# Performance work log

Measured on AMD Instinct MI355X. Metric: run time of the kernel, lower is better.

The kernel has to match this reference:

```python
import jax, jax.numpy as jnp
import numpy as np

IN_FEATURES = 256
OUT_FEATURES = 512
NUM_SEGMENTS = 8
GRID_MIN, GRID_MAX = -1.0, 1.0
STEP = (GRID_MAX - GRID_MIN) / NUM_SEGMENTS
LN_EPS = 1e-5


def setup_inputs() -> dict:
    key = jax.random.key(0)
    k1, k2 = jax.random.split(key)
    B = 2048
    x = jax.random.normal(k1, (B, IN_FEATURES), dtype=jnp.float32)
    # Xavier-uniform a_embed, zeros b_embed, as in reset_parameters
    vocab = IN_FEATURES * NUM_SEGMENTS
    limit = float(np.sqrt(6.0 / (vocab + OUT_FEATURES)))
    a_weight = jax.random.uniform(k2, (vocab, OUT_FEATURES), minval=-limit, maxval=limit, dtype=jnp.float32)
    b_weight = jnp.zeros((vocab, OUT_FEATURES), dtype=jnp.float32)
    gamma = jnp.ones((IN_FEATURES,), dtype=jnp.float32)
    beta = jnp.zeros((IN_FEATURES,), dtype=jnp.float32)
    return {"x": x, "a_weight": a_weight, "b_weight": b_weight, "gamma": gamma, "beta": beta}


def reference(x, a_weight, b_weight, gamma, beta):
    # LayerNorm over in_features
    mu = jnp.mean(x, axis=-1, keepdims=True)
    var = jnp.mean(jnp.square(x - mu), axis=-1, keepdims=True)
    xn = (x - mu) * jax.lax.rsqrt(var + LN_EPS) * gamma + beta  # [B, I]

    # data-dependent segment index (torch .long() truncates; clamp makes trunc==floor here)
    float_idx = (xn - GRID_MIN) / STEP
    seg = jnp.clip(float_idx.astype(jnp.int32), 0, NUM_SEGMENTS - 1)  # [B, I]
    global_idx = seg + jnp.arange(IN_FEATURES, dtype=jnp.int32)[None, :] * NUM_SEGMENTS

    a_vals = a_weight[global_idx]  # [B, I, O]
    b_vals = b_weight[global_idx]  # [B, I, O]
    # sum over in_features of a*x + b
    y = jnp.einsum('bi,bio->bo', xn, a_vals) + jnp.sum(b_vals, axis=1)
    return y
```

## Files before the change

kernel.cpp:

```cpp
#include <hip/hip_runtime.h>

#define I_FEAT 256
#define O_FEAT 512
#define NSEG   8
#define KDIM   (I_FEAT * NSEG)
#define KTOT   (2 * KDIM)
#define KC_N   (KTOT / 32)

typedef _Float16 half8   __attribute__((ext_vector_type(8)));
typedef float    floatx4 __attribute__((ext_vector_type(4)));
typedef uint32_t uintx4  __attribute__((ext_vector_type(4)));

__global__ __launch_bounds__(256) void prep(
    const float* __restrict__ x,
    const float* __restrict__ Aw,
    const float* __restrict__ Bw,
    const float* __restrict__ gamma,
    const float* __restrict__ beta,
    uint4* __restrict__ Bf,
    uint2* __restrict__ Am,
    int Bn, int pbTot)
{
    __shared__ char smem[16 * 260 * 4];
    const int t   = threadIdx.x;
    const int bid = blockIdx.x;

    if (bid < pbTot) {
        unsigned short (*T)[72] = (unsigned short(*)[72])smem;
        const int n0 = (bid & 7) * 64;
        const int k0 = (bid >> 3) * 64;
        const float* src = (k0 < KDIM) ? (Aw + (size_t)k0 * O_FEAT)
                                       : (Bw + (size_t)(k0 - KDIM) * O_FEAT);
        #pragma unroll
        for (int s = 0; s < 4; ++s) {
            int e  = s * 1024 + t * 4;
            int kl = e >> 6, nl = e & 63;
            const float4 v = *(const float4*)(src + (size_t)kl * O_FEAT + n0 + nl);
            T[nl + 0][kl] = __builtin_bit_cast(unsigned short, (_Float16)v.x);
            T[nl + 1][kl] = __builtin_bit_cast(unsigned short, (_Float16)v.y);
            T[nl + 2][kl] = __builtin_bit_cast(unsigned short, (_Float16)v.z);
            T[nl + 3][kl] = __builtin_bit_cast(unsigned short, (_Float16)v.w);
        }
        __syncthreads();

        const int lane = t & 63, lane16 = lane & 15, quad = lane >> 4;
        const int sub  = t >> 6;
        #pragma unroll
        for (int f = 0; f < 2; ++f) {
            const int combo = sub * 2 + f;
            const int n16g  = combo & 3;
            const int kch   = combo >> 2;
            const int nl = n16g * 16 + lane16;
            const int kl = kch * 32 + quad * 8;
            const uint4 val = *(const uint4*)&T[nl][kl];
            const int n16t = (n0 >> 4) + n16g;
            const int kc   = (k0 >> 5) + kch;
            Bf[((size_t)n16t * KC_N + kc) * 64 + lane] = val;
        }
    } else {
        uint32_t (*M)[260] = (uint32_t(*)[260])smem;
        const int mt16 = bid - pbTot;
        const int rr   = t >> 4;
        const int c16  = t & 15;
        const int row  = mt16 * 16 + rr;
        const bool ok  = (row < Bn);

        float4 v[4];
        const float* xr = x + (size_t)row * I_FEAT + c16 * 16;
        #pragma unroll
        for (int j = 0; j < 4; ++j)
            v[j] = ok ? *(const float4*)(xr + j * 4) : make_float4(0.f, 0.f, 0.f, 0.f);

        float sum = 0.f, sq = 0.f;
        #pragma unroll
        for (int j = 0; j < 4; ++j) {
            sum += v[j].x + v[j].y + v[j].z + v[j].w;
            sq  += v[j].x * v[j].x + v[j].y * v[j].y
                 + v[j].z * v[j].z + v[j].w * v[j].w;
        }
        #pragma unroll
        for (int mask = 1; mask < 16; mask <<= 1) {
            sum += __shfl_xor(sum, mask);
            sq  += __shfl_xor(sq,  mask);
        }
        const float mu  = sum * (1.0f / I_FEAT);
        const float var = sq * (1.0f / I_FEAT) - mu * mu;
        const float rs  = rsqrtf(var + 1e-5f);

        #pragma unroll
        for (int j = 0; j < 4; ++j) {
            const float4 g4 = *(const float4*)(gamma + c16 * 16 + j * 4);
            const float4 b4 = *(const float4*)(beta  + c16 * 16 + j * 4);
            const float vv[4] = { v[j].x, v[j].y, v[j].z, v[j].w };
            const float gg[4] = { g4.x, g4.y, g4.z, g4.w };
            const float bb[4] = { b4.x, b4.y, b4.z, b4.w };
            #pragma unroll
            for (int e = 0; e < 4; ++e) {
                const int c = c16 * 16 + j * 4 + e;
                float xn = (vv[e] - mu) * rs * gg[e] + bb[e];
                float fi = (xn + 1.0f) * 4.0f;
                int seg = (int)fi;
                seg = seg < 0 ? 0 : (seg > NSEG - 1 ? NSEG - 1 : seg);
                _Float16 hx = (_Float16)xn;
                M[rr][c] = ((uint32_t)seg << 16)
                         | (uint32_t)__builtin_bit_cast(unsigned short, hx);
            }
        }
        __syncthreads();

        const int lane = t & 63, g = t >> 6;
        const int m_local = lane & 15, quad = lane >> 4;
        uint2* dst = Am + (size_t)mt16 * 64 * 64 + lane;
        #pragma unroll
        for (int kk = 0; kk < 16; ++kk) {
            const int kcp = g * 16 + kk;
            const int w0  = kcp * 8 + quad;
            const int w1  = w0 + 4;
            const uint32_t u0 = M[m_local][w0 & 255];
            const uint32_t u1 = M[m_local][w1 & 255];
            const uint32_t a  = (w0 >> 8) ? ((u0 & 0xFFFF0000u) | 0x3C00u) : u0;
            const uint32_t b  = (w1 >> 8) ? ((u1 & 0xFFFF0000u) | 0x3C00u) : u1;
            dst[(size_t)kcp * 64] = make_uint2(a, b);
        }
    }
}

static __device__ __forceinline__ half8 build_onehot(uint32_t u) {
    const uint32_t xb  = u & 0xFFFFu;
    const uint32_t seg = u >> 16;
    const uint64_t oh  = (uint64_t)xb << ((seg & 3u) << 4);
    const uint64_t lo  = (seg < 4u) ? oh : 0ull;
    const uint64_t hi  = (seg < 4u) ? 0ull : oh;
    uintx4 w;
    w[0] = (uint32_t)lo; w[1] = (uint32_t)(lo >> 32);
    w[2] = (uint32_t)hi; w[3] = (uint32_t)(hi >> 32);
    return __builtin_bit_cast(half8, w);
}

__global__ __launch_bounds__(256, 2) void kan_gemm(
    const uint2* __restrict__ Am,
    const uint4* __restrict__ Bf,
    float* __restrict__ out,
    int Bn, int rt64Tot)
{
    __shared__ floatx4 s_red[4][8][64];

    const int t      = threadIdx.x;
    const int wave   = t >> 6, lane = t & 63;
    const int lane16 = lane & 15, quad = lane >> 4;
    const int bid    = blockIdx.x;

    int ot, rt;
    if (rt64Tot == 32) {
        const int xc = bid & 7, j = bid >> 3;
        ot = ((j >> 4) << 2) | (xc & 3);
        rt = (j & 15) | ((xc >> 2) << 4);
    } else {
        ot = bid & 15;
        rt = bid >> 4;
    }

    const uint2* pa = Am + (size_t)(rt * 4) * 64 * 64 + lane;
    const uint4* pb = Bf + (size_t)(ot * 2) * KC_N * 64 + lane;

    floatx4 acc[4][2] = {};
    const int kcp0 = wave * 16;

    #pragma unroll 4
    for (int p = 0; p < 16; ++p) {
        const int kcp = kcp0 + p;
        const uint2 u0 = pa[(size_t)kcp * 64];
        const uint2 u1 = pa[(size_t)(4096  + kcp * 64)];
        const uint2 u2 = pa[(size_t)(8192  + kcp * 64)];
        const uint2 u3 = pa[(size_t)(12288 + kcp * 64)];
        const uint4 b00 = pb[(size_t)(2 * kcp + 0) * 64];
        const uint4 b01 = pb[(size_t)(2 * kcp + 1) * 64];
        const uint4 b10 = pb[(size_t)(8192 + (2 * kcp + 0) * 64)];
        const uint4 b11 = pb[(size_t)(8192 + (2 * kcp + 1) * 64)];
        {
            const half8 n0 = __builtin_bit_cast(half8, b00);
            const half8 n1 = __builtin_bit_cast(half8, b10);
            half8 a;
            a = build_onehot(u0.x);
            acc[0][0] = __builtin_amdgcn_mfma_f32_16x16x32_f16(a, n0, acc[0][0], 0, 0, 0);
            acc[0][1] = __builtin_amdgcn_mfma_f32_16x16x32_f16(a, n1, acc[0][1], 0, 0, 0);
            a = build_onehot(u1.x);
            acc[1][0] = __builtin_amdgcn_mfma_f32_16x16x32_f16(a, n0, acc[1][0], 0, 0, 0);
            acc[1][1] = __builtin_amdgcn_mfma_f32_16x16x32_f16(a, n1, acc[1][1], 0, 0, 0);
            a = build_onehot(u2.x);
            acc[2][0] = __builtin_amdgcn_mfma_f32_16x16x32_f16(a, n0, acc[2][0], 0, 0, 0);
            acc[2][1] = __builtin_amdgcn_mfma_f32_16x16x32_f16(a, n1, acc[2][1], 0, 0, 0);
            a = build_onehot(u3.x);
            acc[3][0] = __builtin_amdgcn_mfma_f32_16x16x32_f16(a, n0, acc[3][0], 0, 0, 0);
            acc[3][1] = __builtin_amdgcn_mfma_f32_16x16x32_f16(a, n1, acc[3][1], 0, 0, 0);
        }
        {
            const half8 n0 = __builtin_bit_cast(half8, b01);
            const half8 n1 = __builtin_bit_cast(half8, b11);
            half8 a;
            a = build_onehot(u0.y);
            acc[0][0] = __builtin_amdgcn_mfma_f32_16x16x32_f16(a, n0, acc[0][0], 0, 0, 0);
            acc[0][1] = __builtin_amdgcn_mfma_f32_16x16x32_f16(a, n1, acc[0][1], 0, 0, 0);
            a = build_onehot(u1.y);
            acc[1][0] = __builtin_amdgcn_mfma_f32_16x16x32_f16(a, n0, acc[1][0], 0, 0, 0);
            acc[1][1] = __builtin_amdgcn_mfma_f32_16x16x32_f16(a, n1, acc[1][1], 0, 0, 0);
            a = build_onehot(u2.y);
            acc[2][0] = __builtin_amdgcn_mfma_f32_16x16x32_f16(a, n0, acc[2][0], 0, 0, 0);
            acc[2][1] = __builtin_amdgcn_mfma_f32_16x16x32_f16(a, n1, acc[2][1], 0, 0, 0);
            a = build_onehot(u3.y);
            acc[3][0] = __builtin_amdgcn_mfma_f32_16x16x32_f16(a, n0, acc[3][0], 0, 0, 0);
            acc[3][1] = __builtin_amdgcn_mfma_f32_16x16x32_f16(a, n1, acc[3][1], 0, 0, 0);
        }
    }

    #pragma unroll
    for (int mi = 0; mi < 4; ++mi)
        #pragma unroll
        for (int ni = 0; ni < 2; ++ni)
            s_red[wave][mi * 2 + ni][lane] = acc[mi][ni];
    __syncthreads();

    #pragma unroll
    for (int q = 0; q < 2; ++q) {
        const int tt = wave * 2 + q;
        const int mi = tt >> 1, ni = tt & 1;
        floatx4 vsum = s_red[0][tt][lane];
        vsum += s_red[1][tt][lane];
        vsum += s_red[2][tt][lane];
        vsum += s_red[3][tt][lane];
        const int gcol = ot * 32 + ni * 16 + lane16;
        const int gr0  = rt * 64 + mi * 16 + quad * 4;
        #pragma unroll
        for (int r = 0; r < 4; ++r) {
            const int grow = gr0 + r;
            if (grow < Bn)
                out[(size_t)grow * O_FEAT + gcol] = vsum[r];
        }
    }
}

extern "C" void kernel_launch(void* const* d_in, const int* in_sizes, int n_in,
                              void* d_out, int out_size, void* d_ws, size_t ws_size,
                              hipStream_t stream) {
    const float* x   = (const float*)d_in[0];
    const float* Aw  = (const float*)d_in[1];
    const float* Bw  = (const float*)d_in[2];
    const float* gam = (const float*)d_in[3];
    const float* bet = (const float*)d_in[4];
    float* out       = (float*)d_out;

    const int Bn      = in_sizes[0] / I_FEAT;
    const int mt16Tot = (Bn + 15) / 16;
    const int rt64Tot = (Bn + 63) / 64;
    const int pbTot   = (O_FEAT / 64) * (KTOT / 64);

    uint4* Bf = (uint4*)d_ws;
    uint2* Am = (uint2*)(Bf + (size_t)(O_FEAT / 16) * KC_N * 64);

    hipLaunchKernelGGL(prep, dim3(pbTot + mt16Tot), dim3(256), 0, stream,
                       x, Aw, Bw, gam, bet, Bf, Am, Bn, pbTot);
    hipLaunchKernelGGL(kan_gemm, dim3(16 * rt64Tot), dim3(256), 0, stream,
                       Am, Bf, out, Bn, rt64Tot);
}
```

Before: 87.82 us.

## Restructure KAN GEMM with LDS double-buffered B tiles via global_load_lds

Rewrites the GEMM kernel from a split-K design (4 waves each covering a K quarter, then an LDS reduction) to 8 waves sharing a 64x64 output tile. B fragments are staged into double-buffered LDS with async global_load_lds, and A one-hot words are register-prefetched. This aims to cut redundant global B traffic and drop the final cross-wave reduction. In exchange it adds per-stage barriers, fewer MFMAs per wave between loads, and an 8x32 grid instead of 512 1D blocks.

```diff
diff --git a/kernel.cpp b/kernel.cpp
--- a/kernel.cpp
+++ b/kernel.cpp
@@ -21,7 +21,7 @@
     uint2* __restrict__ Am,
     int Bn, int pbTot)
 {
-    __shared__ char smem[16 * 260 * 4];
+    __shared__ uint32_t smem[16 * 260];
     const int t   = threadIdx.x;
     const int bid = blockIdx.x;
 
@@ -137,104 +137,82 @@
     return __builtin_bit_cast(half8, w);
 }
 
-__global__ __launch_bounds__(256, 2) void kan_gemm(
+__global__ __launch_bounds__(512, 2) void kan_gemm(
     const uint2* __restrict__ Am,
     const uint4* __restrict__ Bf,
     float* __restrict__ out,
-    int Bn, int rt64Tot)
+    int Bn)
 {
-    __shared__ floatx4 s_red[4][8][64];
+    __shared__ uint4 bbuf[2][32][64];
 
     const int t      = threadIdx.x;
     const int wave   = t >> 6, lane = t & 63;
+    const int wm     = wave >> 1;
+    const int wn     = wave & 1;
     const int lane16 = lane & 15, quad = lane >> 4;
-    const int bid    = blockIdx.x;
-
-    int ot, rt;
-    if (rt64Tot == 32) {
-        const int xc = bid & 7, j = bid >> 3;
-        ot = ((j >> 4) << 2) | (xc & 3);
-        rt = (j & 15) | ((xc >> 2) << 4);
-    } else {
-        ot = bid & 15;
-        rt = bid >> 4;
+
+    const int nb = blockIdx.x;
+    const int mb = blockIdx.y;
+
+    const uint2* pa = Am + ((size_t)(mb * 4 + wm) * 64) * 64 + lane;
+
+    floatx4 acc0 = {}, acc1 = {};
+
+    auto stage = [&](int s, int b) {
+        const int kc0 = s * 8;
+        #pragma unroll
+        for (int j = 0; j < 4; ++j) {
+            const int idx  = j * 8 + wave;
+            const int n16l = idx >> 3, kcl = idx & 7;
+            const uint4* g = Bf
+                + ((size_t)((nb * 4 + n16l) * KC_N + kc0 + kcl)) * 64 + lane;
+            __builtin_amdgcn_global_load_lds(
+                (const __attribute__((address_space(1))) uint32_t*)g,
+                (__attribute__((address_space(3))) uint32_t*)&bbuf[b][idx][lane],
+                16, 0, 0);
+        }
+    };
+
+    uint2 cur[4], nxt[4];
+    stage(0, 0);
+    #pragma unroll
+    for (int c = 0; c < 4; ++c) cur[c] = pa[(size_t)c * 64];
+    __syncthreads();
+
+    for (int s = 0; s < 16; ++s) {
+        const int b = s & 1;
+        if (s < 15) {
+            stage(s + 1, b ^ 1);
+            #pragma unroll
+            for (int c = 0; c < 4; ++c) nxt[c] = pa[(size_t)((s + 1) * 4 + c) * 64];
+        }
+        #pragma unroll
+        for (int c = 0; c < 4; ++c) {
+            const int kcl0 = c * 2;
+            const half8 b00 = __builtin_bit_cast(half8, bbuf[b][(wn * 2 + 0) * 8 + kcl0][lane]);
+            const half8 b10 = __builtin_bit_cast(half8, bbuf[b][(wn * 2 + 1) * 8 + kcl0][lane]);
+            const half8 b01 = __builtin_bit_cast(half8, bbuf[b][(wn * 2 + 0) * 8 + kcl0 + 1][lane]);
+            const half8 b11 = __builtin_bit_cast(half8, bbuf[b][(wn * 2 + 1) * 8 + kcl0 + 1][lane]);
+            half8 a = build_onehot(cur[c].x);
+            acc0 = __builtin_amdgcn_mfma_f32_16x16x32_f16(a, b00, acc0, 0, 0, 0);
+            acc1 = __builtin_amdgcn_mfma_f32_16x16x32_f16(a, b10, acc1, 0, 0, 0);
+            a = build_onehot(cur[c].y);
+            acc0 = __builtin_amdgcn_mfma_f32_16x16x32_f16(a, b01, acc0, 0, 0, 0);
+            acc1 = __builtin_amdgcn_mfma_f32_16x16x32_f16(a, b11, acc1, 0, 0, 0);
+        }
+        __syncthreads();
+        #pragma unroll
+        for (int c = 0; c < 4; ++c) cur[c] = nxt[c];
     }
 
-    const uint2* pa = Am + (size_t)(rt * 4) * 64 * 64 + lane;
-    const uint4* pb = Bf + (size_t)(ot * 2) * KC_N * 64 + lane;
-
-    floatx4 acc[4][2] = {};
-    const int kcp0 = wave * 16;
-
-    #pragma unroll 4
-    for (int p = 0; p < 16; ++p) {
-        const int kcp = kcp0 + p;
-        const uint2 u0 = pa[(size_t)kcp * 64];
-        const uint2 u1 = pa[(size_t)(4096  + kcp * 64)];
-        const uint2 u2 = pa[(size_t)(8192  + kcp * 64)];
-        const uint2 u3 = pa[(size_t)(12288 + kcp * 64)];
-        const uint4 b00 = pb[(size_t)(2 * kcp + 0) * 64];
-        const uint4 b01 = pb[(size_t)(2 * kcp + 1) * 64];
-        const uint4 b10 = pb[(size_t)(8192 + (2 * kcp + 0) * 64)];
-        const uint4 b11 = pb[(size_t)(8192 + (2 * kcp + 1) * 64)];
-        {
-            const half8 n0 = __builtin_bit_cast(half8, b00);
-            const half8 n1 = __builtin_bit_cast(half8, b10);
-            half8 a;
-            a = build_onehot(u0.x);
-            acc[0][0] = __builtin_amdgcn_mfma_f32_16x16x32_f16(a, n0, acc[0][0], 0, 0, 0);
-            acc[0][1] = __builtin_amdgcn_mfma_f32_16x16x32_f16(a, n1, acc[0][1], 0, 0, 0);
-            a = build_onehot(u1.x);
-            acc[1][0] = __builtin_amdgcn_mfma_f32_16x16x32_f16(a, n0, acc[1][0], 0, 0, 0);
-            acc[1][1] = __builtin_amdgcn_mfma_f32_16x16x32_f16(a, n1, acc[1][1], 0, 0, 0);
-            a = build_onehot(u2.x);
-            acc[2][0] = __builtin_amdgcn_mfma_f32_16x16x32_f16(a, n0, acc[2][0], 0, 0, 0);
-            acc[2][1] = __builtin_amdgcn_mfma_f32_16x16x32_f16(a, n1, acc[2][1], 0, 0, 0);
-            a = build_onehot(u3.x);
-            acc[3][0] = __builtin_amdgcn_mfma_f32_16x16x32_f16(a, n0, acc[3][0], 0, 0, 0);
-            acc[3][1] = __builtin_amdgcn_mfma_f32_16x16x32_f16(a, n1, acc[3][1], 0, 0, 0);
-        }
-        {
-            const half8 n0 = __builtin_bit_cast(half8, b01);
-            const half8 n1 = __builtin_bit_cast(half8, b11);
-            half8 a;
-            a = build_onehot(u0.y);
-            acc[0][0] = __builtin_amdgcn_mfma_f32_16x16x32_f16(a, n0, acc[0][0], 0, 0, 0);
-            acc[0][1] = __builtin_amdgcn_mfma_f32_16x16x32_f16(a, n1, acc[0][1], 0, 0, 0);
-            a = build_onehot(u1.y);
-            acc[1][0] = __builtin_amdgcn_mfma_f32_16x16x32_f16(a, n0, acc[1][0], 0, 0, 0);
-            acc[1][1] = __builtin_amdgcn_mfma_f32_16x16x32_f16(a, n1, acc[1][1], 0, 0, 0);
-            a = build_onehot(u2.y);
-            acc[2][0] = __builtin_amdgcn_mfma_f32_16x16x32_f16(a, n0, acc[2][0], 0, 0, 0);
-            acc[2][1] = __builtin_amdgcn_mfma_f32_16x16x32_f16(a, n1, acc[2][1], 0, 0, 0);
-            a = build_onehot(u3.y);
-            acc[3][0] = __builtin_amdgcn_mfma_f32_16x16x32_f16(a, n0, acc[3][0], 0, 0, 0);
-            acc[3][1] = __builtin_amdgcn_mfma_f32_16x16x32_f16(a, n1, acc[3][1], 0, 0, 0);
-        }
-    }
-
+    const int grow0 = mb * 64 + wm * 16 + quad * 4;
+    const int gcol  = nb * 64 + wn * 32 + lane16;
     #pragma unroll
-    for (int mi = 0; mi < 4; ++mi)
-        #pragma unroll
-        for (int ni = 0; ni < 2; ++ni)
-            s_red[wave][mi * 2 + ni][lane] = acc[mi][ni];
-    __syncthreads();
-
-    #pragma unroll
-    for (int q = 0; q < 2; ++q) {
-        const int tt = wave * 2 + q;
-        const int mi = tt >> 1, ni = tt & 1;
-        floatx4 vsum = s_red[0][tt][lane];
-        vsum += s_red[1][tt][lane];
-        vsum += s_red[2][tt][lane];
-        vsum += s_red[3][tt][lane];
-        const int gcol = ot * 32 + ni * 16 + lane16;
-        const int gr0  = rt * 64 + mi * 16 + quad * 4;
-        #pragma unroll
-        for (int r = 0; r < 4; ++r) {
-            const int grow = gr0 + r;
-            if (grow < Bn)
-                out[(size_t)grow * O_FEAT + gcol] = vsum[r];
+    for (int r = 0; r < 4; ++r) {
+        const int grow = grow0 + r;
+        if (grow < Bn) {
+            out[(size_t)grow * O_FEAT + gcol]      = acc0[r];
+            out[(size_t)grow * O_FEAT + gcol + 16] = acc1[r];
         }
     }
 }
@@ -251,7 +229,7 @@
 
     const int Bn      = in_sizes[0] / I_FEAT;
     const int mt16Tot = (Bn + 15) / 16;
-    const int rt64Tot = (Bn + 63) / 64;
+    const int mb64Tot = (Bn + 63) / 64;
     const int pbTot   = (O_FEAT / 64) * (KTOT / 64);
 
     uint4* Bf = (uint4*)d_ws;
@@ -259,6 +237,6 @@
 
     hipLaunchKernelGGL(prep, dim3(pbTot + mt16Tot), dim3(256), 0, stream,
                        x, Aw, Bw, gam, bet, Bf, Am, Bn, pbTot);
-    hipLaunchKernelGGL(kan_gemm, dim3(16 * rt64Tot), dim3(256), 0, stream,
-                       Am, Bf, out, Bn, rt64Tot);
-}
+    hipLaunchKernelGGL(kan_gemm, dim3(O_FEAT / 64, mb64Tot), dim3(512), 0, stream,
+                       Am, Bf, out, Bn);
+}
```

Result: no change. 89.00 us (+1.3%).
